# Performance work log

Measured on AMD Instinct MI355X. Metric: run time of the kernel, lower is better.

Reference implementation:

```python
import jax, jax.numpy as jnp
import numpy as np

B, S, K, D = 2048, 32, 1024, 64
DECAY = 0.9
LOG_2PI = float(np.log(2.0 * np.pi))


def _gmm_log_probs(slots, mu, log_sigma):
    """log N(slots | mu_k, sigma_k) summed over feature dim -> [B, S, K].

    Expanded quadratic form avoids materializing the [B,S,K,D] broadcast:
    -0.5 * sum_d (x-mu)^2/var - sum_d log sigma - 0.5*D*log(2*pi)
    """
    inv_var = jnp.exp(-2.0 * log_sigma)                      # [K, D]
    x2 = jnp.einsum('bsd,kd->bsk', slots * slots, inv_var)    # sum x^2/var
    xm = jnp.einsum('bsd,kd->bsk', slots, mu * inv_var)       # sum x*mu/var
    m2 = jnp.sum(mu * mu * inv_var, axis=-1)                  # [K]
    const = jnp.sum(log_sigma, axis=-1) + 0.5 * D * LOG_2PI   # [K]
    return -0.5 * (x2 - 2.0 * xm + m2) - const


def setup_inputs() -> dict:
    key = jax.random.key(0)
    k0, k1, k2, k3 = jax.random.split(key, 4)
    return {
        'slots': jax.random.normal(k0, (B, S, D), dtype=jnp.float32),
        'mu': jax.random.normal(k1, (K, D), dtype=jnp.float32),
        'log_sigma': jax.random.normal(k2, (K, D), dtype=jnp.float32),
        'log_prior': jnp.zeros((K,), dtype=jnp.float32),
        'z': jax.random.normal(k3, (B, S, D), dtype=jnp.float32),
    }


def reference(slots, mu, log_sigma, log_prior, z):
    sigma = jnp.exp(log_sigma)                                # [K, D]
    log_probs = _gmm_log_probs(slots, mu, log_sigma)          # [B, S, K]
    responsibilities = jax.nn.softmax(log_probs, axis=-1)     # [B, S, K]
    # argmax of responsibilities == argmax of log_probs (softmax is monotone)
    assignments = jnp.argmax(log_probs, axis=-1)              # [B, S] int
    new_slots = mu[assignments] + sigma[assignments] * z      # [B, S, D]
    log_likelihood = jnp.take_along_axis(
        log_probs, assignments[..., None], axis=-1)[..., 0]   # [B, S]
    # EMA prior update (non-trainable buffer in the original module)
    new_log_prior = (DECAY * jax.nn.softmax(log_prior)
                     + (1.0 - DECAY) * jax.nn.softmax(
                         jnp.sum(responsibilities, axis=(0, 1))))
    return new_slots, log_likelihood, new_log_prior
```

## Files before the change

### kernel.cpp

```cpp
#include <hip/hip_runtime.h>
#include <math.h>

#define KK 1024
#define DD 64
#define BS 65536
#define TM 32
#define NBLK (BS/TM)
#define NTHR 512
#define LN_2PI 1.8378770664093453f
#define DECAY 0.9f
#define APAD 136

typedef _Float16 f16x8 __attribute__((ext_vector_type(8)));
typedef _Float16 f16x4 __attribute__((ext_vector_type(4)));
typedef float f32x16 __attribute__((ext_vector_type(16)));

#define BH_OFF   0
#define BL_OFF   65536
#define C_OFF    131072
#define SIG_OFF  (C_OFF + KK)
#define RESP_OFF (SIG_OFF + KK*DD)

__global__ __launch_bounds__(64) void prep_kernel(
    const float* __restrict__ mu, const float* __restrict__ log_sigma,
    float* __restrict__ ws) {
  int k = blockIdx.x;
  int d = threadIdx.x;
  float ls = log_sigma[k*DD + d];
  float m  = mu[k*DD + d];
  float iv = expf(-2.0f*ls);
  _Float16* Bh = (_Float16*)(ws + BH_OFF);
  _Float16* Bl = (_Float16*)(ws + BL_OFF);
  {
    float w0 = -0.5f*iv;
    _Float16 hh = (_Float16)w0;
    Bh[((size_t)(d >> 3)*KK + k)*8 + (d & 7)] = hh;
    Bl[((size_t)(d >> 3)*KK + k)*8 + (d & 7)] = (_Float16)(w0 - (float)hh);
  }
  {
    float w1 = m*iv;
    _Float16 hh = (_Float16)w1;
    int dd = 64 + d;
    Bh[((size_t)(dd >> 3)*KK + k)*8 + (dd & 7)] = hh;
    Bl[((size_t)(dd >> 3)*KK + k)*8 + (dd & 7)] = (_Float16)(w1 - (float)hh);
  }
  ws[SIG_OFF + k*DD + d] = expf(ls);
  float t1 = m*m*iv;
  float t2 = ls;
  #pragma unroll
  for (int off = 32; off; off >>= 1) {
    t1 += __shfl_xor(t1, off);
    t2 += __shfl_xor(t2, off);
  }
  if (d == 0) ws[C_OFF + k] = -0.5f*t1 - t2 - 32.0f*LN_2PI;
}

__global__ __launch_bounds__(512, 4) void main_kernel(
    const float* __restrict__ slots, const float* __restrict__ mu,
    const float* __restrict__ z, const float* __restrict__ ws,
    float* __restrict__ out_slots, float* __restrict__ out_ll,
    float* __restrict__ resp_g) {
  __shared__ _Float16 Ah[TM][APAD];
  __shared__ _Float16 Al[TM][APAD];
  __shared__ float mxl[TM][8];
  __shared__ float sml[TM][8];
  __shared__ float gm_l[TM];
  __shared__ float inv_l[TM];
  __shared__ int   am_l[TM];

  const int t    = threadIdx.x;
  const int lane = t & 63;
  const int w    = t >> 6;
  const int h    = lane >> 5;
  const int lc   = lane & 31;
  const int R0   = blockIdx.x * TM;

  {
    int row = t >> 4;
    int dp  = (t & 15) * 4;
    float4 v = *(const float4*)(slots + (size_t)(R0 + row)*DD + dp);
    float f[4] = {v.x, v.y, v.z, v.w};
    f16x4 sqh, sql, sh, sl;
    #pragma unroll
    for (int j = 0; j < 4; ++j) {
      float sq = f[j]*f[j];
      _Float16 h1 = (_Float16)sq;
      sqh[j] = h1; sql[j] = (_Float16)(sq - (float)h1);
      _Float16 h2 = (_Float16)f[j];
      sh[j] = h2;  sl[j]  = (_Float16)(f[j] - (float)h2);
    }
    *(f16x4*)&Ah[row][dp]      = sqh;
    *(f16x4*)&Al[row][dp]      = sql;
    *(f16x4*)&Ah[row][64 + dp] = sh;
    *(f16x4*)&Al[row][64 + dp] = sl;
  }
  if (t < TM) am_l[t] = 0x7fffffff;
  __syncthreads();

  const f16x8* BH = (const f16x8*)(ws + BH_OFF);
  const f16x8* BL = (const f16x8*)(ws + BL_OFF);
  const int col0 = (w << 7) + lc;
  const f16x8* pH = BH + (size_t)h*KK + col0;
  const f16x8* pL = BL + (size_t)h*KK + col0;

  f32x16 acc[4];
  {
    const float* Cc = ws + C_OFF;
    #pragma unroll
    for (int ct = 0; ct < 4; ++ct) {
      float cv = Cc[col0 + ct*32];
      f32x16 ini;
      #pragma unroll
      for (int j = 0; j < 16; ++j) ini[j] = cv;
      acc[ct] = ini;
    }
  }

  #pragma unroll
  for (int s = 0; s < 8; ++s) {
    f16x8 ah = *(const f16x8*)&Ah[lc][s*16 + h*8];
    f16x8 al = *(const f16x8*)&Al[lc][s*16 + h*8];
    #pragma unroll
    for (int ct = 0; ct < 4; ++ct) {
      f16x8 bh = pH[(size_t)s*2*KK + ct*32];
      f16x8 bl = pL[(size_t)s*2*KK + ct*32];
      acc[ct] = __builtin_amdgcn_mfma_f32_32x32x16_f16(ah, bh, acc[ct], 0, 0, 0);
      acc[ct] = __builtin_amdgcn_mfma_f32_32x32x16_f16(ah, bl, acc[ct], 0, 0, 0);
      acc[ct] = __builtin_amdgcn_mfma_f32_32x32x16_f16(al, bh, acc[ct], 0, 0, 0);
    }
  }

  #pragma unroll
  for (int q = 0; q < 16; ++q) {
    float m = fmaxf(fmaxf(acc[0][q], acc[1][q]), fmaxf(acc[2][q], acc[3][q]));
    #pragma unroll
    for (int off = 1; off < 32; off <<= 1)
      m = fmaxf(m, __shfl_xor(m, off));
    if (lc == 0) mxl[(q&3) + 8*(q>>2) + 4*h][w] = m;
  }
  __syncthreads();

  if (t < TM) {
    float m = mxl[t][0];
    #pragma unroll
    for (int g = 1; g < 8; ++g) m = fmaxf(m, mxl[t][g]);
    gm_l[t] = m;
    out_ll[R0 + t] = m;
  }
  __syncthreads();

  #pragma unroll
  for (int q = 0; q < 16; ++q) {
    const int row = (q&3) + 8*(q>>2) + 4*h;
    const float gm = gm_l[row];
    int cand = 0x7fffffff;
    #pragma unroll
    for (int ct = 3; ct >= 0; --ct)
      if (acc[ct][q] == gm) cand = col0 + ct*32;
    if (cand != 0x7fffffff) atomicMin(&am_l[row], cand);
    float sacc = 0.0f;
    #pragma unroll
    for (int ct = 0; ct < 4; ++ct) {
      float e = __expf(acc[ct][q] - gm);
      acc[ct][q] = e;
      sacc += e;
    }
    #pragma unroll
    for (int off = 1; off < 32; off <<= 1) sacc += __shfl_xor(sacc, off);
    if (lc == 0) sml[row][w] = sacc;
  }
  __syncthreads();
  if (t < TM) {
    float ssum = 0.0f;
    #pragma unroll
    for (int g = 0; g < 8; ++g) ssum += sml[t][g];
    inv_l[t] = 1.0f / ssum;
  }
  __syncthreads();

  {
    float rc[4] = {0.0f, 0.0f, 0.0f, 0.0f};
    #pragma unroll
    for (int q = 0; q < 16; ++q) {
      int row = (q&3) + 8*(q>>2) + 4*h;
      float inv = inv_l[row];
      #pragma unroll
      for (int ct = 0; ct < 4; ++ct) rc[ct] += acc[ct][q] * inv;
    }
    #pragma unroll
    for (int ct = 0; ct < 4; ++ct) rc[ct] += __shfl_xor(rc[ct], 32);
    if (lane < 32) {
      #pragma unroll
      for (int ct = 0; ct < 4; ++ct) atomicAdd(resp_g + col0 + ct*32, rc[ct]);
    }
  }

  {
    const int frow = t >> 4;
    const int fdp  = (t & 15) * 4;
    const int fa   = am_l[frow];
    float4 fz = *(const float4*)(z  + (size_t)(R0 + frow)*DD + fdp);
    float4 fm = *(const float4*)(mu + (size_t)fa*DD + fdp);
    float4 fs = *(const float4*)(ws + SIG_OFF + (size_t)fa*DD + fdp);
    float4 o;
    o.x = fmaf(fs.x, fz.x, fm.x); o.y = fmaf(fs.y, fz.y, fm.y);
    o.z = fmaf(fs.z, fz.z, fm.z); o.w = fmaf(fs.w, fz.w, fm.w);
    *(float4*)(out_slots + (size_t)(R0 + frow)*DD + fdp) = o;
  }
}

__device__ __forceinline__ float block_max_1024(float v, float* red) {
  #pragma unroll
  for (int off = 32; off; off >>= 1) v = fmaxf(v, __shfl_xor(v, off));
  int wave = threadIdx.x >> 6, lane = threadIdx.x & 63;
  if (lane == 0) red[wave] = v;
  __syncthreads();
  float m = red[0];
  #pragma unroll
  for (int w = 1; w < 16; ++w) m = fmaxf(m, red[w]);
  __syncthreads();
  return m;
}

__device__ __forceinline__ float block_sum_1024(float v, float* red) {
  #pragma unroll
  for (int off = 32; off; off >>= 1) v += __shfl_xor(v, off);
  int wave = threadIdx.x >> 6, lane = threadIdx.x & 63;
  if (lane == 0) red[wave] = v;
  __syncthreads();
  float s = 0.0f;
  #pragma unroll
  for (int w = 0; w < 16; ++w) s += red[w];
  __syncthreads();
  return s;
}

__global__ __launch_bounds__(1024) void finalize_kernel(
    const float* __restrict__ log_prior, const float* __restrict__ resp_g,
    float* __restrict__ out_prior) {
  __shared__ float red[16];
  int t = threadIdx.x;
  float lp = log_prior[t];
  float rs = resp_g[t];

  float m1 = block_max_1024(lp, red);
  float e1 = __expf(lp - m1);
  float s1 = block_sum_1024(e1, red);

  float m2 = block_max_1024(rs, red);
  float e2 = __expf(rs - m2);
  float s2 = block_sum_1024(e2, red);

  out_prior[t] = DECAY * (e1 / s1) + (1.0f - DECAY) * (e2 / s2);
}

extern "C" void kernel_launch(void* const* d_in, const int* in_sizes, int n_in,
                              void* d_out, int out_size, void* d_ws, size_t ws_size,
                              hipStream_t stream) {
  const float* slots     = (const float*)d_in[0];
  const float* mu        = (const float*)d_in[1];
  const float* log_sigma = (const float*)d_in[2];
  const float* log_prior = (const float*)d_in[3];
  const float* z         = (const float*)d_in[4];

  float* out       = (float*)d_out;
  float* out_slots = out;
  float* out_ll    = out + (size_t)BS*DD;
  float* out_prior = out + (size_t)BS*DD + BS;
  float* ws        = (float*)d_ws;

  hipMemsetAsync(ws + RESP_OFF, 0, KK*sizeof(float), stream);
  prep_kernel<<<KK, 64, 0, stream>>>(mu, log_sigma, ws);
  main_kernel<<<NBLK, NTHR, 0, stream>>>(slots, mu, z, ws, out_slots, out_ll,
                                         ws + RESP_OFF);
  finalize_kernel<<<1, 1024, 0, stream>>>(log_prior, ws + RESP_OFF, out_prior);
}
```

Measured before the change: 115.3 us.

## Stream B operand into LDS with double-buffered async loads, A in registers

```diff
diff --git a/kernel.cpp b/kernel.cpp
--- a/kernel.cpp
+++ b/kernel.cpp
@@ -9,10 +9,8 @@
 #define NTHR 512
 #define LN_2PI 1.8378770664093453f
 #define DECAY 0.9f
-#define APAD 136
 
 typedef _Float16 f16x8 __attribute__((ext_vector_type(8)));
-typedef _Float16 f16x4 __attribute__((ext_vector_type(4)));
 typedef float f32x16 __attribute__((ext_vector_type(16)));
 
 #define BH_OFF   0
@@ -20,6 +18,8 @@
 #define C_OFF    131072
 #define SIG_OFF  (C_OFF + KK)
 #define RESP_OFF (SIG_OFF + KK*DD)
+
+#define SMEM_BYTES (131072 + 1024 + 1024 + 128 + 128 + 128)
 
 __global__ __launch_bounds__(64) void prep_kernel(
     const float* __restrict__ mu, const float* __restrict__ log_sigma,
@@ -55,18 +55,53 @@
   if (d == 0) ws[C_OFF + k] = -0.5f*t1 - t2 - 32.0f*LN_2PI;
 }
 
-__global__ __launch_bounds__(512, 4) void main_kernel(
+#define GLD16(g, l) __builtin_amdgcn_global_load_lds( \
+    (const __attribute__((address_space(1))) void*)(g), \
+    (__attribute__((address_space(3))) void*)(l), 16, 0, 0)
+
+#define STAGE(s) do { \
+  const char* _sh = wsB0 + (size_t)(s)*32768; \
+  const char* _sl = wsB1 + (size_t)(s)*32768; \
+  char* _d = Bbase + (((s)&1) ? 65536 : 0); \
+  _Pragma("unroll") \
+  for (int _r = 0; _r < 4; ++_r) { \
+    const int _o = (_r*512 + t)*16; \
+    GLD16(_sh + _o, _d + _o); \
+    GLD16(_sl + _o, _d + 32768 + _o); \
+  } \
+} while (0)
+
+#define ITER(s, VN) do { \
+  asm volatile("s_waitcnt vmcnt(" #VN ")" ::: "memory"); \
+  __builtin_amdgcn_s_barrier(); \
+  asm volatile("" ::: "memory"); \
+  const _Float16* _bp = (const _Float16*)(Bbase + (((s)&1) ? 65536 : 0)); \
+  _Pragma("unroll") \
+  for (int ct = 0; ct < 4; ++ct) { \
+    f16x8 bh = *(const f16x8*)&_bp[(size_t)((h << 10) + col0 + ct*32) * 8]; \
+    f16x8 bl = *(const f16x8*)&_bp[16384 + (size_t)((h << 10) + col0 + ct*32) * 8]; \
+    acc[ct] = __builtin_amdgcn_mfma_f32_32x32x16_f16(Ahreg[(s)], bh, acc[ct], 0, 0, 0); \
+    acc[ct] = __builtin_amdgcn_mfma_f32_32x32x16_f16(Ahreg[(s)], bl, acc[ct], 0, 0, 0); \
+    acc[ct] = __builtin_amdgcn_mfma_f32_32x32x16_f16(Alreg[(s)], bh, acc[ct], 0, 0, 0); \
+  } \
+  asm volatile("" ::: "memory"); \
+  __builtin_amdgcn_s_barrier(); \
+  asm volatile("" ::: "memory"); \
+  if ((s) + 2 < 8) STAGE((s) + 2); \
+} while (0)
+
+__global__ __launch_bounds__(512, 2) void main_kernel(
     const float* __restrict__ slots, const float* __restrict__ mu,
     const float* __restrict__ z, const float* __restrict__ ws,
     float* __restrict__ out_slots, float* __restrict__ out_ll,
     float* __restrict__ resp_g) {
-  __shared__ _Float16 Ah[TM][APAD];
-  __shared__ _Float16 Al[TM][APAD];
-  __shared__ float mxl[TM][8];
-  __shared__ float sml[TM][8];
-  __shared__ float gm_l[TM];
-  __shared__ float inv_l[TM];
-  __shared__ int   am_l[TM];
+  extern __shared__ char smem[];
+  char*  Bbase = smem;
+  float* mxl   = (float*)(smem + 131072);
+  float* sml   = mxl + 256;
+  float* gm_l  = sml + 256;
+  float* inv_l = gm_l + 32;
+  int*   am_l  = (int*)(inv_l + 32);
 
   const int t    = threadIdx.x;
   const int lane = t & 63;
@@ -74,35 +109,18 @@
   const int h    = lane >> 5;
   const int lc   = lane & 31;
   const int R0   = blockIdx.x * TM;
-
-  {
-    int row = t >> 4;
-    int dp  = (t & 15) * 4;
-    float4 v = *(const float4*)(slots + (size_t)(R0 + row)*DD + dp);
-    float f[4] = {v.x, v.y, v.z, v.w};
-    f16x4 sqh, sql, sh, sl;
-    #pragma unroll
-    for (int j = 0; j < 4; ++j) {
-      float sq = f[j]*f[j];
-      _Float16 h1 = (_Float16)sq;
-      sqh[j] = h1; sql[j] = (_Float16)(sq - (float)h1);
-      _Float16 h2 = (_Float16)f[j];
-      sh[j] = h2;  sl[j]  = (_Float16)(f[j] - (float)h2);
-    }
-    *(f16x4*)&Ah[row][dp]      = sqh;
-    *(f16x4*)&Al[row][dp]      = sql;
-    *(f16x4*)&Ah[row][64 + dp] = sh;
-    *(f16x4*)&Al[row][64 + dp] = sl;
-  }
-  if (t < TM) am_l[t] = 0x7fffffff;
-  __syncthreads();
-
-  const f16x8* BH = (const f16x8*)(ws + BH_OFF);
-  const f16x8* BL = (const f16x8*)(ws + BL_OFF);
   const int col0 = (w << 7) + lc;
-  const f16x8* pH = BH + (size_t)h*KK + col0;
-  const f16x8* pL = BL + (size_t)h*KK + col0;
-
+
+  const char* wsB0 = (const char*)ws;
+  const char* wsB1 = (const char*)ws + 262144;
+
+  const float* arow = slots + (size_t)(R0 + lc)*DD + h*8;
+  float4 a0[4], a1[4];
+  #pragma unroll
+  for (int a = 0; a < 4; ++a) {
+    a0[a] = *(const float4*)(arow + a*16);
+    a1[a] = *(const float4*)(arow + a*16 + 4);
+  }
   f32x16 acc[4];
   {
     const float* Cc = ws + C_OFF;
@@ -115,20 +133,33 @@
       acc[ct] = ini;
     }
   }
-
-  #pragma unroll
-  for (int s = 0; s < 8; ++s) {
-    f16x8 ah = *(const f16x8*)&Ah[lc][s*16 + h*8];
-    f16x8 al = *(const f16x8*)&Al[lc][s*16 + h*8];
-    #pragma unroll
-    for (int ct = 0; ct < 4; ++ct) {
-      f16x8 bh = pH[(size_t)s*2*KK + ct*32];
-      f16x8 bl = pL[(size_t)s*2*KK + ct*32];
-      acc[ct] = __builtin_amdgcn_mfma_f32_32x32x16_f16(ah, bh, acc[ct], 0, 0, 0);
-      acc[ct] = __builtin_amdgcn_mfma_f32_32x32x16_f16(ah, bl, acc[ct], 0, 0, 0);
-      acc[ct] = __builtin_amdgcn_mfma_f32_32x32x16_f16(al, bh, acc[ct], 0, 0, 0);
-    }
-  }
+  STAGE(0);
+  STAGE(1);
+
+  float av[32];
+  #pragma unroll
+  for (int a = 0; a < 4; ++a) {
+    av[8*a+0] = a0[a].x; av[8*a+1] = a0[a].y; av[8*a+2] = a0[a].z; av[8*a+3] = a0[a].w;
+    av[8*a+4] = a1[a].x; av[8*a+5] = a1[a].y; av[8*a+6] = a1[a].z; av[8*a+7] = a1[a].w;
+  }
+  f16x8 Ahreg[8], Alreg[8];
+  #pragma unroll
+  for (int s = 0; s < 4; ++s) {
+    #pragma unroll
+    for (int j = 0; j < 8; ++j) {
+      float x = av[8*s + j];
+      float sq = x * x;
+      _Float16 h1 = (_Float16)sq;
+      Ahreg[s][j] = h1;  Alreg[s][j] = (_Float16)(sq - (float)h1);
+      _Float16 h2 = (_Float16)x;
+      Ahreg[s+4][j] = h2; Alreg[s+4][j] = (_Float16)(x - (float)h2);
+    }
+  }
+  if (t < TM) am_l[t] = 0x7fffffff;
+  asm volatile("s_waitcnt lgkmcnt(0)" ::: "memory");
+
+  ITER(0, 8); ITER(1, 8); ITER(2, 8); ITER(3, 8);
+  ITER(4, 8); ITER(5, 8); ITER(6, 8); ITER(7, 0);
 
   #pragma unroll
   for (int q = 0; q < 16; ++q) {
@@ -136,14 +167,14 @@
     #pragma unroll
     for (int off = 1; off < 32; off <<= 1)
       m = fmaxf(m, __shfl_xor(m, off));
-    if (lc == 0) mxl[(q&3) + 8*(q>>2) + 4*h][w] = m;
+    if (lc == 0) mxl[((q&3) + 8*(q>>2) + 4*h)*8 + w] = m;
   }
   __syncthreads();
 
   if (t < TM) {
-    float m = mxl[t][0];
-    #pragma unroll
-    for (int g = 1; g < 8; ++g) m = fmaxf(m, mxl[t][g]);
+    float m = mxl[t*8];
+    #pragma unroll
+    for (int g = 1; g < 8; ++g) m = fmaxf(m, mxl[t*8 + g]);
     gm_l[t] = m;
     out_ll[R0 + t] = m;
   }
@@ -167,13 +198,13 @@
     }
     #pragma unroll
     for (int off = 1; off < 32; off <<= 1) sacc += __shfl_xor(sacc, off);
-    if (lc == 0) sml[row][w] = sacc;
+    if (lc == 0) sml[row*8 + w] = sacc;
   }
   __syncthreads();
   if (t < TM) {
     float ssum = 0.0f;
     #pragma unroll
-    for (int g = 0; g < 8; ++g) ssum += sml[t][g];
+    for (int g = 0; g < 8; ++g) ssum += sml[t*8 + g];
     inv_l[t] = 1.0f / ssum;
   }
   __syncthreads();
@@ -269,9 +300,13 @@
   float* out_prior = out + (size_t)BS*DD + BS;
   float* ws        = (float*)d_ws;
 
+  (void)hipFuncSetAttribute((const void*)main_kernel,
+                            hipFuncAttributeMaxDynamicSharedMemorySize,
+                            SMEM_BYTES);
+
   hipMemsetAsync(ws + RESP_OFF, 0, KK*sizeof(float), stream);
   prep_kernel<<<KK, 64, 0, stream>>>(mu, log_sigma, ws);
-  main_kernel<<<NBLK, NTHR, 0, stream>>>(slots, mu, z, ws, out_slots, out_ll,
-                                         ws + RESP_OFF);
+  main_kernel<<<NBLK, NTHR, SMEM_BYTES, stream>>>(slots, mu, z, ws, out_slots,
+                                                  out_ll, ws + RESP_OFF);
   finalize_kernel<<<1, 1024, 0, stream>>>(log_prior, ws + RESP_OFF, out_prior);
 }
```

New measurement: 170.0 us. 47.5% more time.
